# Performance work log

Hardware: AMD Instinct MI355X
Metric: run time of the kernel (lower is better)

The kernel has to match this reference:

```python
import jax, jax.numpy as jnp
import numpy as np

D_MODEL = 1024
N_HEADS = 16
D_HEAD = D_MODEL // N_HEADS
D_FF = 4096
MAX_ITERS = 2
B, T = 8, 1024
LN_EPS = 1e-5


def _layernorm(x, g, b):
    m = jnp.mean(x, axis=-1, keepdims=True)
    v = jnp.mean(jnp.square(x - m), axis=-1, keepdims=True)
    return (x - m) * jax.lax.rsqrt(v + LN_EPS) * g + b


def setup_inputs() -> dict:
    key = jax.random.key(0)
    ks = jax.random.split(key, 16)
    s = 0.02
    inp = {
        "z": jax.random.normal(ks[0], (B, T, D_MODEL), dtype=jnp.float32),
        # per-head Q/K/V projections stacked over heads: [H, D, Dh], bias [H, Dh]
        "Wq": jax.random.normal(ks[1], (N_HEADS, D_MODEL, D_HEAD), dtype=jnp.float32) * s,
        "bq": jnp.zeros((N_HEADS, D_HEAD), dtype=jnp.float32),
        "Wk": jax.random.normal(ks[2], (N_HEADS, D_MODEL, D_HEAD), dtype=jnp.float32) * s,
        "bk": jnp.zeros((N_HEADS, D_HEAD), dtype=jnp.float32),
        "Wv": jax.random.normal(ks[3], (N_HEADS, D_MODEL, D_HEAD), dtype=jnp.float32) * s,
        "bv": jnp.zeros((N_HEADS, D_HEAD), dtype=jnp.float32),
        "Wo": jax.random.normal(ks[4], (D_MODEL, D_MODEL), dtype=jnp.float32) * s,
        "bo": jnp.zeros((D_MODEL,), dtype=jnp.float32),
        "W1": jax.random.normal(ks[5], (D_MODEL, D_FF), dtype=jnp.float32) * s,
        "b1": jnp.zeros((D_FF,), dtype=jnp.float32),
        "W2": jax.random.normal(ks[6], (D_FF, D_MODEL), dtype=jnp.float32) * s,
        "b2": jnp.zeros((D_MODEL,), dtype=jnp.float32),
        "g1": jnp.ones((D_MODEL,), dtype=jnp.float32),
        "be1": jnp.zeros((D_MODEL,), dtype=jnp.float32),
        "g2": jnp.ones((D_MODEL,), dtype=jnp.float32),
        "be2": jnp.zeros((D_MODEL,), dtype=jnp.float32),
    }
    return inp


def reference(z, Wq, bq, Wk, bk, Wv, bv, Wo, bo, W1, b1, W2, b2, g1, be1, g2, be2):
    # Controller outputs (alphas/state/aux) are unused by the original forward -> omitted.
    # Dropout is inference-identity.
    scale = 1.0 / jnp.sqrt(jnp.asarray(D_HEAD, dtype=z.dtype))
    z_refined = z
    for _ in range(MAX_ITERS):
        # batched per-head projections: [B,H,T,Dh]
        q = jnp.einsum('btd,hdk->bhtk', z, Wq) + bq[None, :, None, :]
        k = jnp.einsum('btd,hdk->bhtk', z, Wk) + bk[None, :, None, :]
        v = jnp.einsum('btd,hdk->bhtk', z, Wv) + bv[None, :, None, :]
        scores = jnp.einsum('bhtk,bhsk->bhts', q, k) * scale  # [B,H,T,T]
        attn = jax.nn.softmax(scores, axis=-1)
        o = jnp.einsum('bhts,bhsk->bhtk', attn, v)  # [B,H,T,Dh]
        # concat heads in order (matches torch.cat over head list)
        o = jnp.transpose(o, (0, 2, 1, 3)).reshape(z.shape[0], z.shape[1], D_MODEL)
        attn_out = o @ Wo + bo
        z = _layernorm(z + attn_out, g1, be1)
        z_refined = z
        ffn = jnp.maximum(z @ W1 + b1, 0.0) @ W2 + b2
        z = _layernorm(z + ffn, g2, be2)
    return z_refined
```

## Files before the change

kernel.cpp:

```cpp
#include <hip/hip_runtime.h>
#include <hip/hip_bf16.h>

typedef __bf16 bf16t;
typedef bf16t bf16x4 __attribute__((ext_vector_type(4)));
typedef bf16t bf16x8 __attribute__((ext_vector_type(8)));
typedef float f32x4 __attribute__((ext_vector_type(4)));

#define BT 8192
#define TT 1024
#define DM 1024
#define DFF 4096

static __device__ __forceinline__ f32x4 mfma16(bf16x8 a, bf16x8 b, f32x4 c) {
  return __builtin_amdgcn_mfma_f32_16x16x32_bf16(a, b, c, 0, 0, 0);
}
static __device__ __forceinline__ bf16x8 ld8(const bf16t* p0, const bf16t* p1) {
  bf16x4 lo = *(const bf16x4*)p0;
  bf16x4 hi = *(const bf16x4*)p1;
  return __builtin_shufflevector(lo, hi, 0, 1, 2, 3, 4, 5, 6, 7);
}
static __device__ __forceinline__ f32x4 f4zero() {
  f32x4 z = {0.f, 0.f, 0.f, 0.f};
  return z;
}
static __device__ __forceinline__ f32x4 vmax4(f32x4 a, f32x4 b) {
  f32x4 r;
#pragma unroll
  for (int i = 0; i < 4; i++) r[i] = fmaxf(a[i], b[i]);
  return r;
}
static __device__ __forceinline__ void gld16(const bf16t* g, bf16t* l) {
  __builtin_amdgcn_global_load_lds((const __attribute__((address_space(1))) void*)g,
                                   (__attribute__((address_space(3))) void*)l, 16, 0, 0);
}
static __device__ __forceinline__ int cperm(int c) {
  return (c & ~31) + (((c >> 2) & 3) << 3) + (((c >> 4) & 1) << 2) + (c & 3);
}

__global__ __launch_bounds__(256) void cvtz_kernel(const float* __restrict__ in,
                                                   bf16t* __restrict__ outp,
                                                   bf16t* __restrict__ outn, long n) {
  long i = ((long)blockIdx.x * 256 + threadIdx.x) * 4;
  if (i >= n) return;
  f32x4 v = *(const f32x4*)&in[i];
  bf16x4 o = {(bf16t)v[0], (bf16t)v[1], (bf16t)v[2], (bf16t)v[3]};
  *(bf16x4*)&outn[i] = o;
  int lo = (int)(i & 1023);
  long p = (i - lo) + cperm(lo);
  *(bf16x4*)&outp[p] = o;
}

__global__ __launch_bounds__(256) void tcvt_kernel(const float* __restrict__ in,
                                                   bf16t* __restrict__ out, int M, int N) {
  __shared__ float T[64][65];
  const int t = threadIdx.x;
  const int ty = t >> 6, tx = t & 63;
  const long n0 = (long)blockIdx.x * 64, m0 = (long)blockIdx.y * 64;
#pragma unroll
  for (int p = 0; p < 16; ++p) {
    int a = ty * 16 + p;
    T[a][tx] = in[(m0 + a) * N + n0 + tx];
  }
  __syncthreads();
#pragma unroll
  for (int p = 0; p < 16; ++p) {
    int r = ty * 16 + p;
    out[(n0 + r) * M + m0 + cperm(tx)] = (bf16t)T[tx][r];
  }
}

__global__ __launch_bounds__(256) void vtrans_kernel(const bf16t* __restrict__ qkv,
                                                     bf16t* __restrict__ vT) {
  __shared__ bf16t T[64][72];
  const int bh = blockIdx.x;
  const int b = bh >> 4, h = bh & 15;
  const int tt = blockIdx.y;
  const int t = threadIdx.x;
  const int ty = t >> 6, tx = t & 63;
  const long srcbase = ((long)b * TT + tt * 64) * 3072 + 2048 + h * 64;
#pragma unroll
  for (int p = 0; p < 16; ++p) {
    int a = ty * 16 + p;
    T[a][tx] = qkv[srcbase + (long)a * 3072 + tx];
  }
  __syncthreads();
  const long dstbase = ((long)bh * 64) * 1024 + tt * 64;
#pragma unroll
  for (int p = 0; p < 16; ++p) {
    int d = ty * 16 + p;
    vT[dstbase + (long)d * 1024 + tx] = T[tx][d];
  }
}

__global__ __launch_bounds__(256) void pack_qkv_t_kernel(const float* __restrict__ Wq,
                                                         const float* __restrict__ Wk,
                                                         const float* __restrict__ Wv,
                                                         bf16t* __restrict__ WT) {
  __shared__ float T[64][65];
  const int bx = blockIdx.x;
  const int sel = bx >> 4, h = bx & 15;
  const float* src = ((sel == 0) ? Wq : (sel == 1) ? Wk : Wv) + (long)h * 65536;
  const long nbase = (long)sel * 1024 + h * 64;
  const long m0 = (long)blockIdx.y * 64;
  const int t = threadIdx.x;
  const int ty = t >> 6, tx = t & 63;
#pragma unroll
  for (int p = 0; p < 16; ++p) {
    int a = ty * 16 + p;
    T[a][tx] = src[(m0 + a) * 64 + tx];
  }
  __syncthreads();
#pragma unroll
  for (int p = 0; p < 16; ++p) {
    int r = ty * 16 + p;
    WT[(nbase + r) * 1024 + m0 + cperm(tx)] = (bf16t)T[tx][r];
  }
}

__global__ __launch_bounds__(256) void pack_bias_kernel(const float* __restrict__ bq,
                                                        const float* __restrict__ bk,
                                                        const float* __restrict__ bv,
                                                        float* __restrict__ bqkv) {
  int i = blockIdx.x * 256 + threadIdx.x;
  if (i >= 3072) return;
  int sel = i >> 10, c = i & 1023;
  bqkv[i] = ((sel == 0) ? bq : (sel == 1) ? bk : bv)[c];
}

template <int EPI>
__global__ __launch_bounds__(256) void gemm_kernel(
    const bf16t* __restrict__ A, const bf16t* __restrict__ Bt,
    const float* __restrict__ bias, const bf16t* __restrict__ resid,
    void* __restrict__ Cout, int M, int N, int K) {
  __shared__ __align__(16) bf16t As[3 * 128 * 32];
  __shared__ __align__(16) bf16t Bs[3 * 128 * 32];
  const int tid = threadIdx.x;
  const int lane = tid & 63;
  const int wid = tid >> 6;
  const int wr = wid >> 1, wc = wid & 1;
  const int g = lane >> 4, lr = lane & 15;

  const int gy = M >> 7;
  const int nwg = gridDim.x;
  const int chunk = nwg >> 3;
  const int wg = blockIdx.x;
  const int lid = (wg & 7) * chunk + (wg >> 3);
  const int gsz = gy << 3;
  const int group = lid / gsz;
  const int rem = lid - group * gsz;
  const int rr = rem >> 3;
  const int cc = (group << 3) + (rem & 7);
  const long brow = (long)rr * 128;
  const long bcol = (long)cc * 128;

  f32x4 acc[4][4];
#pragma unroll
  for (int i = 0; i < 4; i++)
#pragma unroll
    for (int j = 0; j < 4; j++) acc[i][j] = f4zero();

  const int srow = tid >> 2;
  const int csrc = (tid & 3) ^ ((tid >> 3) & 3);
  const bf16t* gA = &A[(brow + srow) * (long)K + 8 * csrc];
  const bf16t* gB = &Bt[(bcol + srow) * (long)K + 8 * csrc];
  bf16t* lA = As + wid * 512;
  bf16t* lB = Bs + wid * 512;

  auto stage = [&](int buf, int k0) {
    gld16(gA + k0, lA + buf * 4096);
    gld16(gA + k0 + (long)64 * K, lA + buf * 4096 + 2048);
    gld16(gB + k0, lB + buf * 4096);
    gld16(gB + k0 + (long)64 * K, lB + buf * 4096 + 2048);
  };
  auto ldf = [&](const bf16t* buf, int row) -> bf16x8 {
    return *(const bf16x8*)(buf + row * 32 + ((((row >> 1) ^ g) & 3) << 3));
  };

  const int nt = K >> 5;
  stage(0, 0);
  stage(1, 32);
  asm volatile("s_waitcnt vmcnt(4)" ::: "memory");
  __builtin_amdgcn_s_barrier();
  __builtin_amdgcn_sched_barrier(0);

  for (int t = 0; t < nt; ++t) {
    const int k2 = (t + 2) << 5;
    const bool pf = (k2 < K);
    if (pf) stage((t + 2) % 3, k2);

    const bf16t* bufA = As + (t % 3) * 4096;
    const bf16t* bufB = Bs + (t % 3) * 4096;
    bf16x8 af[4], bfv[4];
#pragma unroll
    for (int i = 0; i < 4; i++) af[i] = ldf(bufA, wr * 64 + i * 16 + lr);
#pragma unroll
    for (int j = 0; j < 4; j++) bfv[j] = ldf(bufB, wc * 64 + j * 16 + lr);
#pragma unroll
    for (int i = 0; i < 4; i++)
#pragma unroll
      for (int j = 0; j < 4; j++) acc[i][j] = mfma16(af[i], bfv[j], acc[i][j]);

    if (t + 1 < nt) {
      if (pf)
        asm volatile("s_waitcnt vmcnt(4)" ::: "memory");
      else
        asm volatile("s_waitcnt vmcnt(0)" ::: "memory");
      __builtin_amdgcn_s_barrier();
      __builtin_amdgcn_sched_barrier(0);
    }
  }

#pragma unroll
  for (int j = 0; j < 4; j++) {
    int col = (int)bcol + wc * 64 + j * 16 + lr;
    float bval = bias ? bias[col] : 0.f;
#pragma unroll
    for (int i = 0; i < 4; i++) {
      long row0 = brow + wr * 64 + i * 16 + 4 * g;
#pragma unroll
      for (int r2 = 0; r2 < 4; r2++) {
        long row = row0 + r2;
        float v = acc[i][j][r2] + bval;
        if (EPI == 0) {
          ((bf16t*)Cout)[row * N + col] = (bf16t)v;
        } else if (EPI == 1) {
          ((bf16t*)Cout)[row * N + cperm(col)] = (bf16t)fmaxf(v, 0.f);
        } else {
          ((bf16t*)Cout)[row * N + col] = (bf16t)(v + (float)resid[row * N + col]);
        }
      }
    }
  }
}

__global__ __launch_bounds__(256) void attn_kernel(const bf16t* __restrict__ qkv,
                                                   const bf16t* __restrict__ vT,
                                                   bf16t* __restrict__ o) {
  const int bh = blockIdx.x;
  const int b = bh >> 4, h = bh & 15;
  const int qt = blockIdx.y;
  const int tid = threadIdx.x;
  const int lane = tid & 63;
  const int w = tid >> 6;
  const int g = lane >> 4, lr = lane & 15;

  __shared__ __align__(16) bf16t Qs[64 * 64];
  __shared__ __align__(16) bf16t Ks[2][64 * 64];
  __shared__ __align__(16) bf16t Vs[2][64 * 64];

  const long rowbase = (long)b * TT;
  const long qrow0 = rowbase + (long)qt * 64;

  const int srow_in_call = w * 8 + (lane >> 3);
  const int schunk = (lane & 7) ^ ((lane >> 3) & 7);
  const int soff = 8 * schunk;

  const bf16t* qsrc = &qkv[(qrow0 + srow_in_call) * 3072 + h * 64 + soff];
  const bf16t* ksrc = &qkv[(rowbase + srow_in_call) * 3072 + 1024 + h * 64 + soff];
  const bf16t* vsrc = &vT[((long)bh * 64 + srow_in_call) * 1024 + soff];
  bf16t* ldst = (bf16t*)((w * 8) * 64);

  auto stageQ = [&]() {
    gld16(qsrc, Qs + (size_t)ldst);
    gld16(qsrc + (long)32 * 3072, Qs + (size_t)ldst + 32 * 64);
  };
  auto stageK = [&](int buf, int kt) {
    const bf16t* s = ksrc + (long)kt * 64 * 3072;
    gld16(s, Ks[buf] + (size_t)ldst);
    gld16(s + (long)32 * 3072, Ks[buf] + (size_t)ldst + 32 * 64);
  };
  auto stageV = [&](int buf, int kt) {
    const bf16t* s = vsrc + kt * 64;
    gld16(s, Vs[buf] + (size_t)ldst);
    gld16(s + (long)32 * 1024, Vs[buf] + (size_t)ldst + 32 * 64);
  };

  stageQ();
  stageK(0, 0);
  stageV(0, 0);
  __syncthreads();

  const int swk = (lr & 7) << 3;
  const int o0 = (4 * g) ^ swk, o1 = (16 + 4 * g) ^ swk;
  const int o2 = (32 + 4 * g) ^ swk, o3 = (48 + 4 * g) ^ swk;

  const bf16t* qrow = Qs + (w * 16 + lr) * 64;
  const bf16x8 qb_lo = ld8(qrow + o0, qrow + o1);
  const bf16x8 qb_hi = ld8(qrow + o2, qrow + o3);

  f32x4 acc_o[4];
#pragma unroll
  for (int j = 0; j < 4; j++) acc_o[j] = f4zero();
  float mrun = -1e30f, lrun = 0.f;

  int cur = 0;
  for (int kt = 0; kt < 16; ++kt) {
    if (kt < 15) {
      stageK(cur ^ 1, kt + 1);
      stageV(cur ^ 1, kt + 1);
    }

    f32x4 s[4];
#pragma unroll
    for (int jt = 0; jt < 4; jt++) {
      const bf16t* krow = Ks[cur] + (jt * 16 + lr) * 64;
      bf16x8 ka_lo = ld8(krow + o0, krow + o1);
      bf16x8 ka_hi = ld8(krow + o2, krow + o3);
      f32x4 t = f4zero();
      t = mfma16(ka_lo, qb_lo, t);
      t = mfma16(ka_hi, qb_hi, t);
      s[jt] = t;
    }

#pragma unroll
    for (int jt = 0; jt < 4; jt++)
#pragma unroll
      for (int r = 0; r < 4; r++) s[jt][r] *= 0.125f;

    f32x4 mv = vmax4(vmax4(s[0], s[1]), vmax4(s[2], s[3]));
    float tm = fmaxf(fmaxf(mv[0], mv[1]), fmaxf(mv[2], mv[3]));
    tm = fmaxf(tm, __shfl_xor(tm, 16, 64));
    tm = fmaxf(tm, __shfl_xor(tm, 32, 64));

    float mnew = fmaxf(mrun, tm);
    float corr = __expf(mrun - mnew);
    mrun = mnew;

    f32x4 sv = f4zero();
#pragma unroll
    for (int jt = 0; jt < 4; jt++)
#pragma unroll
      for (int r = 0; r < 4; r++) {
        float pv = __expf(s[jt][r] - mnew);
        s[jt][r] = pv;
        sv[r] += pv;
      }
    float tsum = sv[0] + sv[1] + sv[2] + sv[3];
    tsum += __shfl_xor(tsum, 16, 64);
    tsum += __shfl_xor(tsum, 32, 64);
    lrun = lrun * corr + tsum;

#pragma unroll
    for (int r = 0; r < 4; r++) {
      float cq = __shfl(corr, 20 * g + r, 64);
#pragma unroll
      for (int dt = 0; dt < 4; dt++) acc_o[dt][r] *= cq;
    }

    bf16x8 pa0, pa1;
#pragma unroll
    for (int r = 0; r < 4; r++) {
      pa0[r] = (bf16t)s[0][r];
      pa0[r + 4] = (bf16t)s[1][r];
      pa1[r] = (bf16t)s[2][r];
      pa1[r + 4] = (bf16t)s[3][r];
    }

#pragma unroll
    for (int dt = 0; dt < 4; dt++) {
      const bf16t* vrow = Vs[cur] + (dt * 16 + lr) * 64;
      bf16x8 vb_lo = ld8(vrow + o0, vrow + o1);
      bf16x8 vb_hi = ld8(vrow + o2, vrow + o3);
      acc_o[dt] = mfma16(pa0, vb_lo, acc_o[dt]);
      acc_o[dt] = mfma16(pa1, vb_hi, acc_o[dt]);
    }

    __syncthreads();
    cur ^= 1;
  }

  float inv = 1.0f / lrun;
#pragma unroll
  for (int r = 0; r < 4; r++) {
    float iq = __shfl(inv, 20 * g + r, 64);
    long row = qrow0 + w * 16 + 4 * g + r;
#pragma unroll
    for (int dt = 0; dt < 4; dt++) {
      o[row * (long)DM + cperm(h * 64 + dt * 16 + lr)] = (bf16t)(acc_o[dt][r] * iq);
    }
  }
}

__global__ __launch_bounds__(256) void ln_kernel(const bf16t* __restrict__ x,
                                                 const float* __restrict__ gamma,
                                                 const float* __restrict__ beta,
                                                 bf16t* __restrict__ out_act,
                                                 bf16t* __restrict__ out_res,
                                                 float* __restrict__ out_f32) {
  const long row = blockIdx.x;
  const int tid = threadIdx.x;
  const int idx = tid * 4;
  bf16x4 xv = *(const bf16x4*)&x[row * DM + idx];
  float v[4];
#pragma unroll
  for (int c = 0; c < 4; c++) v[c] = (float)xv[c];
  float s = v[0] + v[1] + v[2] + v[3];
  float ss = v[0] * v[0] + v[1] * v[1] + v[2] * v[2] + v[3] * v[3];
#pragma unroll
  for (int m = 1; m < 64; m <<= 1) {
    s += __shfl_xor(s, m, 64);
    ss += __shfl_xor(ss, m, 64);
  }
  __shared__ float red[8];
  const int w = tid >> 6, lane = tid & 63;
  if (lane == 0) {
    red[w] = s;
    red[4 + w] = ss;
  }
  __syncthreads();
  s = red[0] + red[1] + red[2] + red[3];
  ss = red[4] + red[5] + red[6] + red[7];
  float mean = s * (1.f / DM);
  float var = ss * (1.f / DM) - mean * mean;
  float inv = rsqrtf(var + 1e-5f);
  f32x4 ga = *(const f32x4*)&gamma[idx];
  f32x4 be = *(const f32x4*)&beta[idx];
  float y[4];
#pragma unroll
  for (int c = 0; c < 4; c++) y[c] = (v[c] - mean) * inv * ga[c] + be[c];
  if (out_act) {
    bf16x4 ob = {(bf16t)y[0], (bf16t)y[1], (bf16t)y[2], (bf16t)y[3]};
    *(bf16x4*)&out_act[row * DM + cperm(idx)] = ob;
  }
  if (out_res) {
    bf16x4 ob = {(bf16t)y[0], (bf16t)y[1], (bf16t)y[2], (bf16t)y[3]};
    *(bf16x4*)&out_res[row * DM + idx] = ob;
  }
  if (out_f32) {
    f32x4 of = {y[0], y[1], y[2], y[3]};
    *(f32x4*)&out_f32[row * DM + idx] = of;
  }
}

extern "C" void kernel_launch(void* const* d_in, const int* in_sizes, int n_in,
                              void* d_out, int out_size, void* d_ws, size_t ws_size,
                              hipStream_t stream) {
  const float* z = (const float*)d_in[0];
  const float* Wq = (const float*)d_in[1];
  const float* bq = (const float*)d_in[2];
  const float* Wk = (const float*)d_in[3];
  const float* bk = (const float*)d_in[4];
  const float* Wv = (const float*)d_in[5];
  const float* bv = (const float*)d_in[6];
  const float* Wo = (const float*)d_in[7];
  const float* bo = (const float*)d_in[8];
  const float* W1 = (const float*)d_in[9];
  const float* b1 = (const float*)d_in[10];
  const float* W2 = (const float*)d_in[11];
  const float* b2 = (const float*)d_in[12];
  const float* g1 = (const float*)d_in[13];
  const float* be1 = (const float*)d_in[14];
  const float* g2 = (const float*)d_in[15];
  const float* be2 = (const float*)d_in[16];

  char* p = (char*)d_ws;
  auto alloc = [&](size_t bytes) {
    char* r = p;
    p += (bytes + 255) & ~(size_t)255;
    return r;
  };
  bf16t* wqkvT = (bf16t*)alloc((size_t)3072 * 1024 * 2);
  float* bqkv = (float*)alloc((size_t)3072 * 4);
  bf16t* woT = (bf16t*)alloc((size_t)1024 * 1024 * 2);
  bf16t* w1T = (bf16t*)alloc((size_t)4096 * 1024 * 2);
  bf16t* w2T = (bf16t*)alloc((size_t)1024 * 4096 * 2);
  bf16t* act = (bf16t*)alloc((size_t)BT * 1024 * 2);
  bf16t* zbf = (bf16t*)alloc((size_t)BT * 1024 * 2);
  bf16t* obuf = (bf16t*)alloc((size_t)BT * 1024 * 2);
  bf16t* big = (bf16t*)alloc((size_t)BT * 4096 * 2);
  bf16t* tbuf = (bf16t*)alloc((size_t)BT * 1024 * 2);
  bf16t* residf = (bf16t*)alloc((size_t)BT * 1024 * 2);
  bf16t* vT = (bf16t*)tbuf;

  pack_qkv_t_kernel<<<dim3(48, 16), dim3(256), 0, stream>>>(Wq, Wk, Wv, wqkvT);
  pack_bias_kernel<<<dim3(12), dim3(256), 0, stream>>>(bq, bk, bv, bqkv);
  tcvt_kernel<<<dim3(16, 16), dim3(256), 0, stream>>>(Wo, woT, 1024, 1024);
  tcvt_kernel<<<dim3(64, 16), dim3(256), 0, stream>>>(W1, w1T, 1024, 4096);
  tcvt_kernel<<<dim3(16, 64), dim3(256), 0, stream>>>(W2, w2T, 4096, 1024);
  cvtz_kernel<<<dim3(8192), dim3(256), 0, stream>>>(z, act, zbf, (long)BT * 1024);

  for (int iter = 0; iter < 2; ++iter) {
    gemm_kernel<0><<<dim3(1536), dim3(256), 0, stream>>>(
        act, wqkvT, bqkv, (const bf16t*)nullptr, (void*)big, BT, 3072, 1024);
    vtrans_kernel<<<dim3(128, 16), dim3(256), 0, stream>>>(big, vT);
    attn_kernel<<<dim3(128, 16), dim3(256), 0, stream>>>(big, vT, obuf);
    const bf16t* rsrc = (iter == 0) ? zbf : residf;
    gemm_kernel<2><<<dim3(512), dim3(256), 0, stream>>>(
        obuf, woT, bo, rsrc, (void*)tbuf, BT, 1024, 1024);
    if (iter == 1) {
      ln_kernel<<<dim3(8192), dim3(256), 0, stream>>>(tbuf, g1, be1, (bf16t*)nullptr,
                                                      (bf16t*)nullptr, (float*)d_out);
      break;
    }
    ln_kernel<<<dim3(8192), dim3(256), 0, stream>>>(tbuf, g1, be1, act, residf,
                                                    (float*)nullptr);
    gemm_kernel<1><<<dim3(2048), dim3(256), 0, stream>>>(
        act, w1T, b1, (const bf16t*)nullptr, (void*)big, BT, 4096, 1024);
    gemm_kernel<2><<<dim3(512), dim3(256), 0, stream>>>(
        big, w2T, b2, residf, (void*)tbuf, BT, 1024, 4096);
    ln_kernel<<<dim3(8192), dim3(256), 0, stream>>>(tbuf, g2, be2, act, residf,
                                                    (float*)nullptr);
  }
}
```

Baseline: 622.9 us.

## Permute QKV layout for 16-byte LDS loads, fold scale into Q, lazy rescale

The QKV GEMM epilogue now premultiplies Q by scale*log2(e) and writes Q/K columns in a permuted order, and the V transpose applies the same permutation. This lets the attention kernel read each MFMA operand with a single 16-byte LDS load from a split-half swizzled layout instead of two 8-byte loads. The softmax uses exp2, drops the per-tile scale multiply, and rescales the accumulator only when the running max grows by more than a threshold. The thresholded rescale adds a wave-wide branch and lets unnormalised values grow somewhat, which trades exactness of the running max for fewer shuffles and multiplies.

```diff
diff --git a/kernel.cpp b/kernel.cpp
--- a/kernel.cpp
+++ b/kernel.cpp
@@ -10,14 +10,10 @@
 #define TT 1024
 #define DM 1024
 #define DFF 4096
+#define QSCALE 0.18033688011112042f
 
 static __device__ __forceinline__ f32x4 mfma16(bf16x8 a, bf16x8 b, f32x4 c) {
   return __builtin_amdgcn_mfma_f32_16x16x32_bf16(a, b, c, 0, 0, 0);
-}
-static __device__ __forceinline__ bf16x8 ld8(const bf16t* p0, const bf16t* p1) {
-  bf16x4 lo = *(const bf16x4*)p0;
-  bf16x4 hi = *(const bf16x4*)p1;
-  return __builtin_shufflevector(lo, hi, 0, 1, 2, 3, 4, 5, 6, 7);
 }
 static __device__ __forceinline__ f32x4 f4zero() {
   f32x4 z = {0.f, 0.f, 0.f, 0.f};
@@ -85,10 +81,11 @@
   }
   __syncthreads();
   const long dstbase = ((long)bh * 64) * 1024 + tt * 64;
+  const int txp = cperm(tx);
 #pragma unroll
   for (int p = 0; p < 16; ++p) {
     int d = ty * 16 + p;
-    vT[dstbase + (long)d * 1024 + tx] = T[tx][d];
+    vT[dstbase + (long)d * 1024 + txp] = T[tx][d];
   }
 }
 
@@ -222,7 +219,9 @@
         long row = row0 + r2;
         float v = acc[i][j][r2] + bval;
         if (EPI == 0) {
-          ((bf16t*)Cout)[row * N + col] = (bf16t)v;
+          float vv = (col < 1024) ? v * QSCALE : v;
+          int oc = (col < 2048) ? cperm(col) : col;
+          ((bf16t*)Cout)[row * N + oc] = (bf16t)vv;
         } else if (EPI == 1) {
           ((bf16t*)Cout)[row * N + cperm(col)] = (bf16t)fmaxf(v, 0.f);
         } else {
@@ -244,35 +243,37 @@
   const int w = tid >> 6;
   const int g = lane >> 4, lr = lane & 15;
 
-  __shared__ __align__(16) bf16t Qs[64 * 64];
-  __shared__ __align__(16) bf16t Ks[2][64 * 64];
-  __shared__ __align__(16) bf16t Vs[2][64 * 64];
+  __shared__ __align__(16) bf16t Qs[2 * 64 * 32];
+  __shared__ __align__(16) bf16t Ks[2][2 * 64 * 32];
+  __shared__ __align__(16) bf16t Vs[2][2 * 64 * 32];
 
   const long rowbase = (long)b * TT;
   const long qrow0 = rowbase + (long)qt * 64;
 
-  const int srow_in_call = w * 8 + (lane >> 3);
-  const int schunk = (lane & 7) ^ ((lane >> 3) & 7);
-  const int soff = 8 * schunk;
-
-  const bf16t* qsrc = &qkv[(qrow0 + srow_in_call) * 3072 + h * 64 + soff];
-  const bf16t* ksrc = &qkv[(rowbase + srow_in_call) * 3072 + 1024 + h * 64 + soff];
-  const bf16t* vsrc = &vT[((long)bh * 64 + srow_in_call) * 1024 + soff];
-  bf16t* ldst = (bf16t*)((w * 8) * 64);
+  const int sq = tid >> 2;
+  const int sco = (((tid & 3) ^ ((tid >> 3) & 3))) * 8;
+
+  const bf16t* qsrc = &qkv[(qrow0 + sq) * 3072 + h * 64 + sco];
+  const bf16t* ksrc = &qkv[(rowbase + sq) * 3072 + 1024 + h * 64 + sco];
+  const bf16t* vsrc = &vT[((long)bh * 64 + sq) * 1024 + sco];
+  const int wbase = w * 512;
 
   auto stageQ = [&]() {
-    gld16(qsrc, Qs + (size_t)ldst);
-    gld16(qsrc + (long)32 * 3072, Qs + (size_t)ldst + 32 * 64);
+    gld16(qsrc, Qs + wbase);
+    gld16(qsrc + 32, Qs + 2048 + wbase);
   };
   auto stageK = [&](int buf, int kt) {
     const bf16t* s = ksrc + (long)kt * 64 * 3072;
-    gld16(s, Ks[buf] + (size_t)ldst);
-    gld16(s + (long)32 * 3072, Ks[buf] + (size_t)ldst + 32 * 64);
+    gld16(s, Ks[buf] + wbase);
+    gld16(s + 32, Ks[buf] + 2048 + wbase);
   };
   auto stageV = [&](int buf, int kt) {
     const bf16t* s = vsrc + kt * 64;
-    gld16(s, Vs[buf] + (size_t)ldst);
-    gld16(s + (long)32 * 1024, Vs[buf] + (size_t)ldst + 32 * 64);
+    gld16(s, Vs[buf] + wbase);
+    gld16(s + 32, Vs[buf] + 2048 + wbase);
+  };
+  auto ldf = [&](const bf16t* base, int hh, int row) -> bf16x8 {
+    return *(const bf16x8*)(base + hh * 2048 + row * 32 + ((((row >> 1) ^ g) & 3) << 3));
   };
 
   stageQ();
@@ -280,13 +281,9 @@
   stageV(0, 0);
   __syncthreads();
 
-  const int swk = (lr & 7) << 3;
-  const int o0 = (4 * g) ^ swk, o1 = (16 + 4 * g) ^ swk;
-  const int o2 = (32 + 4 * g) ^ swk, o3 = (48 + 4 * g) ^ swk;
-
-  const bf16t* qrow = Qs + (w * 16 + lr) * 64;
-  const bf16x8 qb_lo = ld8(qrow + o0, qrow + o1);
-  const bf16x8 qb_hi = ld8(qrow + o2, qrow + o3);
+  const int qr = w * 16 + lr;
+  const bf16x8 qb_lo = ldf(Qs, 0, qr);
+  const bf16x8 qb_hi = ldf(Qs, 1, qr);
 
   f32x4 acc_o[4];
 #pragma unroll
@@ -303,49 +300,46 @@
     f32x4 s[4];
 #pragma unroll
     for (int jt = 0; jt < 4; jt++) {
-      const bf16t* krow = Ks[cur] + (jt * 16 + lr) * 64;
-      bf16x8 ka_lo = ld8(krow + o0, krow + o1);
-      bf16x8 ka_hi = ld8(krow + o2, krow + o3);
+      int krow = jt * 16 + lr;
+      bf16x8 ka_lo = ldf(Ks[cur], 0, krow);
+      bf16x8 ka_hi = ldf(Ks[cur], 1, krow);
       f32x4 t = f4zero();
       t = mfma16(ka_lo, qb_lo, t);
       t = mfma16(ka_hi, qb_hi, t);
       s[jt] = t;
     }
 
-#pragma unroll
-    for (int jt = 0; jt < 4; jt++)
-#pragma unroll
-      for (int r = 0; r < 4; r++) s[jt][r] *= 0.125f;
-
     f32x4 mv = vmax4(vmax4(s[0], s[1]), vmax4(s[2], s[3]));
     float tm = fmaxf(fmaxf(mv[0], mv[1]), fmaxf(mv[2], mv[3]));
     tm = fmaxf(tm, __shfl_xor(tm, 16, 64));
     tm = fmaxf(tm, __shfl_xor(tm, 32, 64));
 
-    float mnew = fmaxf(mrun, tm);
-    float corr = __expf(mrun - mnew);
-    mrun = mnew;
+    if (__any(tm > mrun + 11.5f)) {
+      float mnew = fmaxf(mrun, tm);
+      float corr = __builtin_amdgcn_exp2f(mrun - mnew);
+      mrun = mnew;
+      lrun *= corr;
+#pragma unroll
+      for (int r = 0; r < 4; r++) {
+        float cq = __shfl(corr, 20 * g + r, 64);
+#pragma unroll
+        for (int dt = 0; dt < 4; dt++) acc_o[dt][r] *= cq;
+      }
+    }
 
     f32x4 sv = f4zero();
 #pragma unroll
     for (int jt = 0; jt < 4; jt++)
 #pragma unroll
       for (int r = 0; r < 4; r++) {
-        float pv = __expf(s[jt][r] - mnew);
+        float pv = __builtin_amdgcn_exp2f(s[jt][r] - mrun);
         s[jt][r] = pv;
         sv[r] += pv;
       }
     float tsum = sv[0] + sv[1] + sv[2] + sv[3];
     tsum += __shfl_xor(tsum, 16, 64);
     tsum += __shfl_xor(tsum, 32, 64);
-    lrun = lrun * corr + tsum;
-
-#pragma unroll
-    for (int r = 0; r < 4; r++) {
-      float cq = __shfl(corr, 20 * g + r, 64);
-#pragma unroll
-      for (int dt = 0; dt < 4; dt++) acc_o[dt][r] *= cq;
-    }
+    lrun += tsum;
 
     bf16x8 pa0, pa1;
 #pragma unroll
@@ -358,9 +352,9 @@
 
 #pragma unroll
     for (int dt = 0; dt < 4; dt++) {
-      const bf16t* vrow = Vs[cur] + (dt * 16 + lr) * 64;
-      bf16x8 vb_lo = ld8(vrow + o0, vrow + o1);
-      bf16x8 vb_hi = ld8(vrow + o2, vrow + o3);
+      int vrow = dt * 16 + lr;
+      bf16x8 vb_lo = ldf(Vs[cur], 0, vrow);
+      bf16x8 vb_hi = ldf(Vs[cur], 1, vrow);
       acc_o[dt] = mfma16(pa0, vb_lo, acc_o[dt]);
       acc_o[dt] = mfma16(pa1, vb_hi, acc_o[dt]);
     }
```

New measurement: 574.3 us. 7.8% less time.
